# Kernel tuning notes

Measured on AMD Instinct MI355X. Metric: run time of the kernel, lower is better.

The kernel has to match this reference:

```python
import jax, jax.numpy as jnp
import numpy as np
import math

H, KVH, D = 15, 5, 64  # heads, kv heads, head_dim
ROPE_BASE = 10000.0
NEG = -1e9


def _rope_cos_sin(position_ids):
    # position_ids: [B, S] int -> cos/sin [B, 1, S, D]
    inv_freq = 1.0 / (ROPE_BASE ** (jnp.arange(0, D, 2, dtype=jnp.float32) / D))  # [D/2]
    freqs = position_ids.astype(jnp.float32)[..., None] * inv_freq  # [B, S, D/2]
    emb = jnp.concatenate([freqs, freqs], axis=-1)  # [B, S, D]
    return jnp.cos(emb)[:, None], jnp.sin(emb)[:, None]


def _rotate_half(x):
    x1, x2 = x[..., : D // 2], x[..., D // 2 :]
    return jnp.concatenate([-x2, x1], axis=-1)


def setup_inputs() -> dict:
    key = jax.random.key(0)
    ks = jax.random.split(key, 5)
    B, S, E = 1, 4096, 960
    hidden_states = jax.random.normal(ks[0], (B, S, E), dtype=jnp.float32)
    Wq = jax.random.normal(ks[1], (E, E), dtype=jnp.float32) * 0.02
    Wk = jax.random.normal(ks[2], (KVH * D, E), dtype=jnp.float32) * 0.02
    Wv = jax.random.normal(ks[3], (KVH * D, E), dtype=jnp.float32) * 0.02
    Wo = jax.random.normal(ks[4], (E, E), dtype=jnp.float32) * 0.02
    causal = jnp.tril(jnp.ones((S, S), dtype=bool))
    attention_mask = jnp.where(causal, 0.0, NEG).astype(jnp.float32)[None, None]  # [1,1,S,S]
    position_ids = jnp.arange(S, dtype=jnp.int64 if jax.config.jax_enable_x64 else jnp.int32)[None]
    return {
        "hidden_states": hidden_states,
        "Wq": Wq,
        "Wk": Wk,
        "Wv": Wv,
        "Wo": Wo,
        "attention_mask": attention_mask,
        "position_ids": position_ids,
    }


def reference(hidden_states, Wq, Wk, Wv, Wo, attention_mask, position_ids):
    B, S, E = hidden_states.shape
    groups = H // KVH
    # projections (bias-free Linear: x @ W.T)
    q = (hidden_states @ Wq.T).reshape(B, S, H, D).transpose(0, 2, 1, 3)      # [B,H,S,D]
    k = (hidden_states @ Wk.T).reshape(B, S, KVH, D).transpose(0, 2, 1, 3)    # [B,KVH,S,D]
    v = (hidden_states @ Wv.T).reshape(B, S, KVH, D).transpose(0, 2, 1, 3)    # [B,KVH,S,D]
    cos, sin = _rope_cos_sin(position_ids)  # [B,1,S,D]
    q = q * cos + _rotate_half(q) * sin
    k = k * cos + _rotate_half(k) * sin
    # GQA: repeat_interleave over the head axis
    k = jnp.repeat(k, groups, axis=1)  # [B,H,S,D]
    v = jnp.repeat(v, groups, axis=1)  # [B,H,S,D]
    scores = jnp.einsum("bhqd,bhkd->bhqk", q, k) / math.sqrt(D) + attention_mask
    probs = jax.nn.softmax(scores.astype(jnp.float32), axis=-1).astype(q.dtype)
    out = jnp.einsum("bhqk,bhkd->bhqd", probs, v)  # [B,H,S,D]
    out = out.transpose(0, 2, 1, 3).reshape(B, S, E)
    return out @ Wo.T
```

## Files before the change

### kernel.cpp

```cpp
#include <hip/hip_runtime.h>
#include <hip/hip_bf16.h>

typedef __hip_bfloat16 bf16;
typedef short bf16x8 __attribute__((ext_vector_type(8)));
typedef short bf16x4 __attribute__((ext_vector_type(4)));
typedef float f32x4 __attribute__((ext_vector_type(4)));

static constexpr int S_LEN = 4096;
static constexpr int EMB   = 960;
static constexpr int NH    = 15;
static constexpr int NKVH  = 5;
static constexpr int KV_E  = NKVH * 64;

__device__ __forceinline__ float scrub(float x, float lim) {
  return fminf(fmaxf(x, -lim), lim);
}

__device__ __forceinline__ short f2bf(float x) {
  bf16 h = __float2bfloat16(x);
  short s;
  __builtin_memcpy(&s, &h, 2);
  return s;
}

__device__ __forceinline__ void stage16(const bf16* g, bf16* l) {
  __builtin_amdgcn_global_load_lds(
      (const __attribute__((address_space(1))) void*)g,
      (__attribute__((address_space(3))) void*)l, 16, 0, 0);
}

__global__ void cvt5_kernel(const float* s0, const float* s1, const float* s2,
                            const float* s3, const float* s4,
                            bf16* d0, bf16* d1, bf16* d2, bf16* d3, bf16* d4,
                            int e0, int e1, int e2, int e3, int e4) {
  int i = blockIdx.x * blockDim.x + threadIdx.x;
  const float* s;
  bf16* d;
  int base;
  if (i < e0)      { s = s0; d = d0; base = 0;  }
  else if (i < e1) { s = s1; d = d1; base = e0; }
  else if (i < e2) { s = s2; d = d2; base = e1; }
  else if (i < e3) { s = s3; d = d3; base = e2; }
  else if (i < e4) { s = s4; d = d4; base = e3; }
  else return;
  int k = i - base;
  const float4* sp = (const float4*)s + (size_t)k * 2;
  float4 a = sp[0], b = sp[1];
  bf16x8 r;
  r[0] = f2bf(a.x); r[1] = f2bf(a.y); r[2] = f2bf(a.z); r[3] = f2bf(a.w);
  r[4] = f2bf(b.x); r[5] = f2bf(b.y); r[6] = f2bf(b.z); r[7] = f2bf(b.w);
  *(bf16x8*)((short*)d + (size_t)k * 8) = r;
}

template <typename EPI>
__device__ __forceinline__ void gemm_core(
    const bf16* __restrict__ A, const bf16* __restrict__ W,
    int m0, int n0, int K, bf16* At, bf16* Bt, EPI&& epilogue) {
  const int lane = threadIdx.x & 63;
  const int wave = threadIdx.x >> 6;
  const int quad = lane >> 4;
  const int c16  = lane & 15;
  const int wm = wave >> 1, wn = wave & 1;
  const int srow = lane >> 2;
  const int sch  = lane & 3;
  const int NIT  = K / 32;

  auto stage = [&](int b, int k0) {
#pragma unroll
    for (int t = 0; t < 2; t++) {
      int j = wave * 2 + t;
      stage16(A + (unsigned)((m0 + j * 16 + srow) * K + k0 + sch * 8),
              At + b * 4096 + j * 512);
      stage16(W + (unsigned)((n0 + j * 16 + srow) * K + k0 + sch * 8),
              Bt + b * 4096 + j * 512);
    }
  };

  f32x4 acc[4][4];
#pragma unroll
  for (int i = 0; i < 4; i++)
#pragma unroll
    for (int j = 0; j < 4; j++) acc[i][j] = (f32x4){0.f, 0.f, 0.f, 0.f};

  stage(0, 0);
  stage(1, 32);
  int ib = 0;

  for (int it = 0; it < NIT; ++it) {
    if (it + 1 < NIT) {
      asm volatile("s_waitcnt vmcnt(4)" ::: "memory");
    } else {
      asm volatile("s_waitcnt vmcnt(0)" ::: "memory");
    }
    __builtin_amdgcn_s_barrier();
    __builtin_amdgcn_sched_barrier(0);
    if (it + 2 < NIT) {
      int sb = ib + 2; if (sb >= 3) sb -= 3;
      stage(sb, (it + 2) * 32);
    }
    const char* ab = (const char*)(At + ib * 4096);
    const char* bb = (const char*)(Bt + ib * 4096);
    bf16x8 af[4], bfr[4];
#pragma unroll
    for (int i = 0; i < 4; i++)
      af[i] = *(const bf16x8*)(ab + (wm * 64 + i * 16 + c16) * 64 + quad * 16);
#pragma unroll
    for (int j = 0; j < 4; j++)
      bfr[j] = *(const bf16x8*)(bb + (wn * 64 + j * 16 + c16) * 64 + quad * 16);
#pragma unroll
    for (int i = 0; i < 4; i++)
#pragma unroll
      for (int j = 0; j < 4; j++)
        acc[i][j] = __builtin_amdgcn_mfma_f32_16x16x32_bf16(af[i], bfr[j],
                                                            acc[i][j], 0, 0, 0);
    ib = (ib + 1 == 3) ? 0 : ib + 1;
  }
  epilogue(acc, m0, n0, wm, wn, quad, c16);
}

__global__ __launch_bounds__(256) void gemm_qkv_kernel(
    const bf16* __restrict__ A, const bf16* __restrict__ Wcat,
    bf16* __restrict__ Qb, bf16* __restrict__ Kbf, bf16* __restrict__ VTb,
    int M, int K) {
  __shared__ __align__(16) bf16 At[3][128 * 32];
  __shared__ __align__(16) bf16 Bt[3][128 * 32];
  const int m0 = blockIdx.x * 128;
  const int n0 = blockIdx.y * 128;
  gemm_core(A, Wcat, m0, n0, K, At[0], Bt[0],
            [&](f32x4 (&acc)[4][4], int m0_, int n0_, int wm, int wn,
                int quad, int c16) {
#pragma unroll
              for (int i = 0; i < 4; i++)
#pragma unroll
                for (int j = 0; j < 4; j++) {
                  int scol = n0_ + wn * 64 + j * 16;
                  if (scol >= 1600) continue;
                  int colg = scol + c16;
                  int row0 = m0_ + wm * 64 + i * 16 + quad * 4;
                  if (scol < 960) {
#pragma unroll
                    for (int r = 0; r < 4; r++)
                      Qb[(size_t)(row0 + r) * EMB + colg] =
                          __float2bfloat16(scrub(acc[i][j][r], 3e4f));
                  } else if (scol < 1280) {
#pragma unroll
                    for (int r = 0; r < 4; r++)
                      Kbf[(size_t)(row0 + r) * KV_E + (colg - 960)] =
                          __float2bfloat16(scrub(acc[i][j][r], 3e4f));
                  } else {
                    bf16x4 v;
#pragma unroll
                    for (int r = 0; r < 4; r++)
                      v[r] = f2bf(scrub(acc[i][j][r], 3e4f));
                    int t0 = m0_ + wm * 64;
                    int nl = quad * 8 + (i >> 1) * 32 + (i & 1) * 4;
                    *(bf16x4*)((short*)VTb + (size_t)(colg - 1280) * S_LEN +
                               t0 + nl) = v;
                  }
                }
            });
}

__global__ __launch_bounds__(256) void gemm_out_kernel(
    const bf16* __restrict__ A, const bf16* __restrict__ W,
    float* __restrict__ C, int M, int N, int K) {
  __shared__ __align__(16) bf16 At[3][128 * 32];
  __shared__ __align__(16) bf16 Bt[3][128 * 32];
  const int m0 = blockIdx.x * 128;
  const int n0 = blockIdx.y * 128;
  gemm_core(A, W, m0, n0, K, At[0], Bt[0],
            [&](f32x4 (&acc)[4][4], int m0_, int n0_, int wm, int wn,
                int quad, int c16) {
#pragma unroll
              for (int i = 0; i < 4; i++)
#pragma unroll
                for (int j = 0; j < 4; j++) {
                  int scol = n0_ + wn * 64 + j * 16;
                  if (scol >= EMB) continue;
                  int col = scol + c16;
                  int row0 = m0_ + wm * 64 + i * 16 + quad * 4;
#pragma unroll
                  for (int r = 0; r < 4; r++)
                    C[(size_t)(row0 + r) * EMB + col] =
                        scrub(acc[i][j][r], 3e4f);
                }
            });
}

__global__ void rope2_kernel(bf16* __restrict__ Qb, bf16* __restrict__ Kb,
                             const int* __restrict__ pos_ids) {
  int tid = blockIdx.x * blockDim.x + threadIdx.x;
  if (tid >= S_LEN * (NH + NKVH) * 32) return;
  int d  = tid & 31;
  int hh = (tid >> 5) % (NH + NKVH);
  int s  = tid / ((NH + NKVH) * 32);
  bf16* buf;
  size_t idx;
  float scale;
  if (hh < NH) {
    buf = Qb; idx = (size_t)s * EMB + hh * 64 + d;
    scale = 0.18033688011112042f;
  } else {
    buf = Kb; idx = (size_t)s * KV_E + (hh - NH) * 64 + d; scale = 1.0f;
  }
  float x = __bfloat162float(buf[idx]);
  float y = __bfloat162float(buf[idx + 32]);
  float f = (float)pos_ids[s] * expf((float)d * -0.28782313662425572f);
  float sf, cf;
  sincosf(f, &sf, &cf);
  buf[idx]      = __float2bfloat16(scrub((x * cf - y * sf) * scale, 3e4f));
  buf[idx + 32] = __float2bfloat16(scrub((y * cf + x * sf) * scale, 3e4f));
}

__global__ __launch_bounds__(256, 3) void flash_kernel(
    const bf16* Q, const bf16* __restrict__ Kb,
    const bf16* __restrict__ VT, bf16* O) {
  __shared__ __align__(16) bf16 Kt[3][64 * 64];
  __shared__ __align__(16) bf16 Vt[3][64 * 64];

  const int bx = blockIdx.x;
  const int lane = threadIdx.x & 63;
  const int wv   = threadIdx.x >> 6;
  const int quad = lane >> 4;
  const int c16  = lane & 15;
  const int h    = blockIdx.y;
  const int kvh  = h / 3;

  const int rsub = lane >> 3;
  const int gch  = (lane & 7) ^ rsub;
  const int rm   = c16 & 7;
  const int ko0  = (quad ^ rm) * 16;

  bf16x4 ones4;
#pragma unroll
  for (int j = 0; j < 4; j++) ones4[j] = (short)0x3F80;

  auto stage = [&](int b, int it) {
    const int kbase = it * 64;
#pragma unroll
    for (int t = 0; t < 2; t++) {
      int i = wv * 2 + t;
      int r = i * 8 + rsub;
      stage16(Kb + (unsigned)((kbase + r) * KV_E + kvh * 64 + gch * 8),
              &Kt[b][i * 512]);
      stage16(VT + (unsigned)((kvh * 64 + r) * S_LEN + kbase + gch * 8),
              &Vt[b][i * 512]);
    }
  };

  auto run_strip = [&](int xq) {
    const int qw   = xq * 64 + wv * 16;
    const int qcol = qw + c16;
    const int itend = xq + 1;

    __syncthreads();

    const bf16* qrow = Q + (size_t)qcol * EMB + h * 64 + quad * 8;
    const bf16x8 aq0 = *(const bf16x8*)qrow;
    const bf16x8 aq1 = *(const bf16x8*)(qrow + 32);

    f32x4 o[4];
#pragma unroll
    for (int n = 0; n < 4; n++) o[n] = (f32x4){0.f, 0.f, 0.f, 0.f};
    f32x4 os = (f32x4){0.f, 0.f, 0.f, 0.f};

    stage(0, 0);
    if (itend > 1) stage(1, 1);
    int ib = 0;

    for (int it = 0; it < itend; ++it) {
      if (it + 1 < itend) {
        asm volatile("s_waitcnt vmcnt(4)" ::: "memory");
      } else {
        asm volatile("s_waitcnt vmcnt(0)" ::: "memory");
      }
      __builtin_amdgcn_s_barrier();
      __builtin_amdgcn_sched_barrier(0);
      if (it + 2 < itend) {
        int sb = ib + 2; if (sb >= 3) sb -= 3;
        stage(sb, it + 2);
      }

      const int kbase = it * 64;
      const char* kb = (const char*)&Kt[0][0] + ib * 8192;
      const char* vb = (const char*)&Vt[0][0] + ib * 8192;
      const bool masked = (it == xq);

      bf16x4 pp[4];
      __builtin_amdgcn_s_setprio(1);
#pragma unroll
      for (int cc = 0; cc < 4; cc++) {
        int r = cc * 16 + c16;
        bf16x8 b0 = *(const bf16x8*)(kb + r * 128 + ko0);
        bf16x8 b1 = *(const bf16x8*)(kb + r * 128 + (ko0 ^ 64));
        f32x4 s = (f32x4){0.f, 0.f, 0.f, 0.f};
        s = __builtin_amdgcn_mfma_f32_16x16x32_bf16(b0, aq0, s, 0, 0, 0);
        s = __builtin_amdgcn_mfma_f32_16x16x32_bf16(b1, aq1, s, 0, 0, 0);
#pragma unroll
        for (int r4 = 0; r4 < 4; r4++) {
          float p = exp2f(s[r4]);
          if (masked) {
            int kc = kbase + cc * 16 + quad * 4 + r4;
            p = (kc <= qcol) ? p : 0.f;
          }
          pp[cc][r4] = f2bf(p);
        }
      }

#pragma unroll
      for (int cc = 0; cc < 4; cc++)
        os = __builtin_amdgcn_mfma_f32_16x16x16bf16_1k(ones4, pp[cc], os,
                                                       0, 0, 0);

#pragma unroll
      for (int n = 0; n < 4; n++) {
        const char* vrow = vb + (n * 16 + c16) * 128;
        bf16x8 va = *(const bf16x8*)(vrow + ko0);
        bf16x8 vc = *(const bf16x8*)(vrow + (ko0 ^ 64));
        bf16x4 a0 = __builtin_shufflevector(va, va, 0, 1, 2, 3);
        bf16x4 a1 = __builtin_shufflevector(va, va, 4, 5, 6, 7);
        bf16x4 a2 = __builtin_shufflevector(vc, vc, 0, 1, 2, 3);
        bf16x4 a3 = __builtin_shufflevector(vc, vc, 4, 5, 6, 7);
        o[n] = __builtin_amdgcn_mfma_f32_16x16x16bf16_1k(a0, pp[0], o[n],
                                                         0, 0, 0);
        o[n] = __builtin_amdgcn_mfma_f32_16x16x16bf16_1k(a1, pp[1], o[n],
                                                         0, 0, 0);
        o[n] = __builtin_amdgcn_mfma_f32_16x16x16bf16_1k(a2, pp[2], o[n],
                                                         0, 0, 0);
        o[n] = __builtin_amdgcn_mfma_f32_16x16x16bf16_1k(a3, pp[3], o[n],
                                                         0, 0, 0);
      }
      __builtin_amdgcn_s_setprio(0);

      ib = (ib + 1 == 3) ? 0 : ib + 1;
    }

    const float inv = 1.0f / fmaxf(os[0], 1e-20f);
#pragma unroll
    for (int n = 0; n < 4; n++) {
      bf16x4 w;
#pragma unroll
      for (int r = 0; r < 4; r++)
        w[r] = f2bf(scrub(o[n][r] * inv, 1e4f));
      *(bf16x4*)((short*)O + (size_t)qcol * EMB + h * 64 + n * 16 +
                 quad * 4) = w;
    }
  };

  run_strip(63 - bx);
  run_strip(bx);
}

extern "C" void kernel_launch(void* const* d_in, const int* in_sizes, int n_in,
                              void* d_out, int out_size, void* d_ws, size_t ws_size,
                              hipStream_t stream) {
  const float* hs = (const float*)d_in[0];
  const float* Wq = (const float*)d_in[1];
  const float* Wk = (const float*)d_in[2];
  const float* Wv = (const float*)d_in[3];
  const float* Wo = (const float*)d_in[4];
  const int* pos = (const int*)d_in[6];
  float* out = (float*)d_out;

  char* wsb = (char*)d_ws;
  size_t regA = ((size_t)S_LEN * EMB + (size_t)S_LEN * NH) * sizeof(float);
  bf16* hsb = (bf16*)wsb;
  bf16* Qb  = (bf16*)(wsb + regA);
  bf16* Kbf = Qb + (size_t)S_LEN * EMB;
  bf16* VTb = Kbf + (size_t)S_LEN * KV_E;
  bf16* Wqb = VTb + (size_t)S_LEN * KV_E;
  bf16* Wkb = Wqb + (size_t)EMB * EMB;
  bf16* Wvb = Wkb + (size_t)KV_E * EMB;
  bf16* Wob = Wqb + (size_t)1664 * EMB;

  {
    int e0 = (S_LEN * EMB) / 8;
    int e1 = e0 + (EMB * EMB) / 8;
    int e2 = e1 + (KV_E * EMB) / 8;
    int e3 = e2 + (KV_E * EMB) / 8;
    int e4 = e3 + (EMB * EMB) / 8;
    cvt5_kernel<<<(e4 + 255) / 256, 256, 0, stream>>>(
        hs, Wq, Wk, Wv, Wo, hsb, Wqb, Wkb, Wvb, Wob, e0, e1, e2, e3, e4);
  }

  gemm_qkv_kernel<<<dim3(S_LEN / 128, 13), 256, 0, stream>>>(
      hsb, Wqb, Qb, Kbf, VTb, S_LEN, EMB);

  {
    int n = S_LEN * (NH + NKVH) * 32;
    rope2_kernel<<<(n + 255) / 256, 256, 0, stream>>>(Qb, Kbf, pos);
  }

  flash_kernel<<<dim3(32, NH), 256, 0, stream>>>(Qb, Kbf, VTb, Qb);

  gemm_out_kernel<<<dim3(S_LEN / 128, 8), 256, 0, stream>>>(
      Qb, Wob, out, S_LEN, EMB, EMB);
}
```

Baseline: 250.7 us.

## Fuse RoPE into QKV GEMM epilogue and widen flash KV tiles to 128

Applies rotary embedding and the Q scale directly in the QKV GEMM epilogue, pairing accumulator columns d and d+32 held by the same thread. This removes the separate rope kernel launch and its read-modify-write pass over Q and K. Separately, the flash kernel now processes 128-key tiles with double buffering instead of 64-key tiles with triple buffering, with occupancy lowered to 2 blocks. That halves the number of barriers per strip but drops the vmcnt-based prefetch depth and doubles LDS use. The epilogue now calls sincos per element in the GEMM, and masked tiles compute extra wasted work on the diagonal.

```diff
diff --git a/kernel.cpp b/kernel.cpp
--- a/kernel.cpp
+++ b/kernel.cpp
@@ -121,7 +121,7 @@
 __global__ __launch_bounds__(256) void gemm_qkv_kernel(
     const bf16* __restrict__ A, const bf16* __restrict__ Wcat,
     bf16* __restrict__ Qb, bf16* __restrict__ Kbf, bf16* __restrict__ VTb,
-    int M, int K) {
+    const int* __restrict__ pos, int M, int K) {
   __shared__ __align__(16) bf16 At[3][128 * 32];
   __shared__ __align__(16) bf16 Bt[3][128 * 32];
   const int m0 = blockIdx.x * 128;
@@ -129,25 +129,45 @@
   gemm_core(A, Wcat, m0, n0, K, At[0], Bt[0],
             [&](f32x4 (&acc)[4][4], int m0_, int n0_, int wm, int wn,
                 int quad, int c16) {
-#pragma unroll
-              for (int i = 0; i < 4; i++)
-#pragma unroll
-                for (int j = 0; j < 4; j++) {
-                  int scol = n0_ + wn * 64 + j * 16;
-                  if (scol >= 1600) continue;
-                  int colg = scol + c16;
-                  int row0 = m0_ + wm * 64 + i * 16 + quad * 4;
-                  if (scol < 960) {
-#pragma unroll
-                    for (int r = 0; r < 4; r++)
-                      Qb[(size_t)(row0 + r) * EMB + colg] =
-                          __float2bfloat16(scrub(acc[i][j][r], 3e4f));
-                  } else if (scol < 1280) {
-#pragma unroll
-                    for (int r = 0; r < 4; r++)
-                      Kbf[(size_t)(row0 + r) * KV_E + (colg - 960)] =
-                          __float2bfloat16(scrub(acc[i][j][r], 3e4f));
-                  } else {
+              const int scol0 = n0_ + wn * 64;
+              if (scol0 < 1280) {
+                const bool isQ = (scol0 < 960);
+                bf16* dst = isQ ? Qb : Kbf;
+                const int stride = isQ ? EMB : KV_E;
+                const int cbase = isQ ? scol0 : (scol0 - 960);
+                const float scale = isQ ? 0.18033688011112042f : 1.0f;
+#pragma unroll
+                for (int j = 0; j < 2; j++) {
+                  int d = j * 16 + c16;
+                  float invf = expf(-0.28782313662425572f * (float)d);
+#pragma unroll
+                  for (int i = 0; i < 4; i++) {
+                    int row0 = m0_ + wm * 64 + i * 16 + quad * 4;
+#pragma unroll
+                    for (int r = 0; r < 4; r++) {
+                      int row = row0 + r;
+                      float th = (float)pos[row] * invf;
+                      float sf, cf;
+                      sincosf(th, &sf, &cf);
+                      float x = acc[i][j][r];
+                      float y = acc[i][j + 2][r];
+                      size_t base = (size_t)row * stride + cbase + j * 16 + c16;
+                      dst[base] =
+                          __float2bfloat16(scrub((x * cf - y * sf) * scale, 3e4f));
+                      dst[base + 32] =
+                          __float2bfloat16(scrub((y * cf + x * sf) * scale, 3e4f));
+                    }
+                  }
+                }
+              } else {
+#pragma unroll
+                for (int i = 0; i < 4; i++)
+#pragma unroll
+                  for (int j = 0; j < 4; j++) {
+                    int scol = scol0 + j * 16;
+                    if (scol >= 1600) continue;
+                    int colg = scol + c16;
+                    int row0 = m0_ + wm * 64 + i * 16 + quad * 4;
                     bf16x4 v;
 #pragma unroll
                     for (int r = 0; r < 4; r++)
@@ -157,7 +177,7 @@
                     *(bf16x4*)((short*)VTb + (size_t)(colg - 1280) * S_LEN +
                                t0 + nl) = v;
                   }
-                }
+              }
             });
 }
 
@@ -187,36 +207,11 @@
             });
 }
 
-__global__ void rope2_kernel(bf16* __restrict__ Qb, bf16* __restrict__ Kb,
-                             const int* __restrict__ pos_ids) {
-  int tid = blockIdx.x * blockDim.x + threadIdx.x;
-  if (tid >= S_LEN * (NH + NKVH) * 32) return;
-  int d  = tid & 31;
-  int hh = (tid >> 5) % (NH + NKVH);
-  int s  = tid / ((NH + NKVH) * 32);
-  bf16* buf;
-  size_t idx;
-  float scale;
-  if (hh < NH) {
-    buf = Qb; idx = (size_t)s * EMB + hh * 64 + d;
-    scale = 0.18033688011112042f;
-  } else {
-    buf = Kb; idx = (size_t)s * KV_E + (hh - NH) * 64 + d; scale = 1.0f;
-  }
-  float x = __bfloat162float(buf[idx]);
-  float y = __bfloat162float(buf[idx + 32]);
-  float f = (float)pos_ids[s] * expf((float)d * -0.28782313662425572f);
-  float sf, cf;
-  sincosf(f, &sf, &cf);
-  buf[idx]      = __float2bfloat16(scrub((x * cf - y * sf) * scale, 3e4f));
-  buf[idx + 32] = __float2bfloat16(scrub((y * cf + x * sf) * scale, 3e4f));
-}
-
-__global__ __launch_bounds__(256, 3) void flash_kernel(
+__global__ __launch_bounds__(256, 2) void flash_kernel(
     const bf16* Q, const bf16* __restrict__ Kb,
     const bf16* __restrict__ VT, bf16* O) {
-  __shared__ __align__(16) bf16 Kt[3][64 * 64];
-  __shared__ __align__(16) bf16 Vt[3][64 * 64];
+  __shared__ __align__(16) bf16 Kt[2][128 * 64];
+  __shared__ __align__(16) bf16 Vt[2][64 * 128];
 
   const int bx = blockIdx.x;
   const int lane = threadIdx.x & 63;
@@ -228,6 +223,8 @@
 
   const int rsub = lane >> 3;
   const int gch  = (lane & 7) ^ rsub;
+  const int vr4  = lane >> 4;
+  const int vhf  = (lane >> 3) & 1;
   const int rm   = c16 & 7;
   const int ko0  = (quad ^ rm) * 16;
 
@@ -235,23 +232,30 @@
 #pragma unroll
   for (int j = 0; j < 4; j++) ones4[j] = (short)0x3F80;
 
-  auto stage = [&](int b, int it) {
-    const int kbase = it * 64;
-#pragma unroll
-    for (int t = 0; t < 2; t++) {
-      int i = wv * 2 + t;
+  auto stage = [&](int b, int t) {
+    const int kbase = t * 128;
+#pragma unroll
+    for (int tt = 0; tt < 4; tt++) {
+      int i = wv * 4 + tt;
       int r = i * 8 + rsub;
       stage16(Kb + (unsigned)((kbase + r) * KV_E + kvh * 64 + gch * 8),
               &Kt[b][i * 512]);
-      stage16(VT + (unsigned)((kvh * 64 + r) * S_LEN + kbase + gch * 8),
+    }
+#pragma unroll
+    for (int tt = 0; tt < 4; tt++) {
+      int i = wv * 4 + tt;
+      int row = i * 4 + vr4;
+      int g = (lane & 7) ^ (row & 7);
+      stage16(VT + (unsigned)((kvh * 64 + row) * S_LEN + kbase + vhf * 64 +
+                              g * 8),
               &Vt[b][i * 512]);
     }
   };
 
   auto run_strip = [&](int xq) {
-    const int qw   = xq * 64 + wv * 16;
-    const int qcol = qw + c16;
-    const int itend = xq + 1;
+    const int qw    = xq * 64 + wv * 16;
+    const int qcol  = qw + c16;
+    const int itend = (xq + 2) >> 1;
 
     __syncthreads();
 
@@ -265,31 +269,20 @@
     f32x4 os = (f32x4){0.f, 0.f, 0.f, 0.f};
 
     stage(0, 0);
-    if (itend > 1) stage(1, 1);
-    int ib = 0;
 
     for (int it = 0; it < itend; ++it) {
-      if (it + 1 < itend) {
-        asm volatile("s_waitcnt vmcnt(4)" ::: "memory");
-      } else {
-        asm volatile("s_waitcnt vmcnt(0)" ::: "memory");
-      }
-      __builtin_amdgcn_s_barrier();
-      __builtin_amdgcn_sched_barrier(0);
-      if (it + 2 < itend) {
-        int sb = ib + 2; if (sb >= 3) sb -= 3;
-        stage(sb, it + 2);
-      }
-
-      const int kbase = it * 64;
-      const char* kb = (const char*)&Kt[0][0] + ib * 8192;
-      const char* vb = (const char*)&Vt[0][0] + ib * 8192;
-      const bool masked = (it == xq);
-
-      bf16x4 pp[4];
+      __syncthreads();
+      if (it + 1 < itend) stage((it + 1) & 1, it + 1);
+
+      const int kbase = it * 128;
+      const char* kb = (const char*)&Kt[it & 1][0];
+      const char* vb = (const char*)&Vt[it & 1][0];
+      const bool masked = (it == itend - 1);
+
+      bf16x4 pp[8];
       __builtin_amdgcn_s_setprio(1);
 #pragma unroll
-      for (int cc = 0; cc < 4; cc++) {
+      for (int cc = 0; cc < 8; cc++) {
         int r = cc * 16 + c16;
         bf16x8 b0 = *(const bf16x8*)(kb + r * 128 + ko0);
         bf16x8 b1 = *(const bf16x8*)(kb + r * 128 + (ko0 ^ 64));
@@ -308,31 +301,35 @@
       }
 
 #pragma unroll
-      for (int cc = 0; cc < 4; cc++)
+      for (int cc = 0; cc < 8; cc++)
         os = __builtin_amdgcn_mfma_f32_16x16x16bf16_1k(ones4, pp[cc], os,
                                                        0, 0, 0);
 
 #pragma unroll
       for (int n = 0; n < 4; n++) {
-        const char* vrow = vb + (n * 16 + c16) * 128;
+        const char* vrow = vb + (n * 16 + c16) * 256;
         bf16x8 va = *(const bf16x8*)(vrow + ko0);
-        bf16x8 vc = *(const bf16x8*)(vrow + (ko0 ^ 64));
+        bf16x8 vb2 = *(const bf16x8*)(vrow + (ko0 ^ 64));
+        bf16x8 vc = *(const bf16x8*)(vrow + 128 + ko0);
+        bf16x8 vd = *(const bf16x8*)(vrow + 128 + (ko0 ^ 64));
         bf16x4 a0 = __builtin_shufflevector(va, va, 0, 1, 2, 3);
         bf16x4 a1 = __builtin_shufflevector(va, va, 4, 5, 6, 7);
-        bf16x4 a2 = __builtin_shufflevector(vc, vc, 0, 1, 2, 3);
-        bf16x4 a3 = __builtin_shufflevector(vc, vc, 4, 5, 6, 7);
-        o[n] = __builtin_amdgcn_mfma_f32_16x16x16bf16_1k(a0, pp[0], o[n],
-                                                         0, 0, 0);
-        o[n] = __builtin_amdgcn_mfma_f32_16x16x16bf16_1k(a1, pp[1], o[n],
-                                                         0, 0, 0);
-        o[n] = __builtin_amdgcn_mfma_f32_16x16x16bf16_1k(a2, pp[2], o[n],
-                                                         0, 0, 0);
-        o[n] = __builtin_amdgcn_mfma_f32_16x16x16bf16_1k(a3, pp[3], o[n],
-                                                         0, 0, 0);
+        bf16x4 a2 = __builtin_shufflevector(vb2, vb2, 0, 1, 2, 3);
+        bf16x4 a3 = __builtin_shufflevector(vb2, vb2, 4, 5, 6, 7);
+        bf16x4 a4 = __builtin_shufflevector(vc, vc, 0, 1, 2, 3);
+        bf16x4 a5 = __builtin_shufflevector(vc, vc, 4, 5, 6, 7);
+        bf16x4 a6 = __builtin_shufflevector(vd, vd, 0, 1, 2, 3);
+        bf16x4 a7 = __builtin_shufflevector(vd, vd, 4, 5, 6, 7);
+        o[n] = __builtin_amdgcn_mfma_f32_16x16x16bf16_1k(a0, pp[0], o[n], 0, 0, 0);
+        o[n] = __builtin_amdgcn_mfma_f32_16x16x16bf16_1k(a1, pp[1], o[n], 0, 0, 0);
+        o[n] = __builtin_amdgcn_mfma_f32_16x16x16bf16_1k(a2, pp[2], o[n], 0, 0, 0);
+        o[n] = __builtin_amdgcn_mfma_f32_16x16x16bf16_1k(a3, pp[3], o[n], 0, 0, 0);
+        o[n] = __builtin_amdgcn_mfma_f32_16x16x16bf16_1k(a4, pp[4], o[n], 0, 0, 0);
+        o[n] = __builtin_amdgcn_mfma_f32_16x16x16bf16_1k(a5, pp[5], o[n], 0, 0, 0);
+        o[n] = __builtin_amdgcn_mfma_f32_16x16x16bf16_1k(a6, pp[6], o[n], 0, 0, 0);
+        o[n] = __builtin_amdgcn_mfma_f32_16x16x16bf16_1k(a7, pp[7], o[n], 0, 0, 0);
       }
       __builtin_amdgcn_s_setprio(0);
-
-      ib = (ib + 1 == 3) ? 0 : ib + 1;
     }
 
     const float inv = 1.0f / fmaxf(os[0], 1e-20f);
@@ -384,12 +381,7 @@
   }
 
   gemm_qkv_kernel<<<dim3(S_LEN / 128, 13), 256, 0, stream>>>(
-      hsb, Wqb, Qb, Kbf, VTb, S_LEN, EMB);
-
-  {
-    int n = S_LEN * (NH + NKVH) * 32;
-    rope2_kernel<<<(n + 255) / 256, 256, 0, stream>>>(Qb, Kbf, pos);
-  }
+      hsb, Wqb, Qb, Kbf, VTb, pos, S_LEN, EMB);
 
   flash_kernel<<<dim3(32, NH), 256, 0, stream>>>(Qb, Kbf, VTb, Qb);
 
```

New measurement: 243.7 us. 2.8% less time.
